# Performance work log

Hardware: AMD Instinct MI355X
Metric: run time of the kernel (lower is better)

Reference implementation:

```python
import jax, jax.numpy as jnp
from jax import lax
import numpy as np

# Module hyperparameters (match init_kwargs)
N = 4            # number of multiplex cells per feature map
NUM_FM = 64      # feature maps in the input
NF = N * NUM_FM  # lateral channel count = 256
H = W = 32       # feature map height/width
D = 2            # lateral neighborhood radius
PRD = 2          # padding repair distance (must equal D for symmetric pad)
KS = 2 * D + 1   # lateral kernel size = 5
IOTA = 0.1       # blend of activation vs lateral support for winner selection
B = 16           # batch size


def minmax_fm(x):
    """Min-max normalize each feature map (over the last two dims) to [0,1].
    Degenerate (constant) maps map to 0."""
    mn = jnp.min(x, axis=(-2, -1), keepdims=True)
    mx = jnp.max(x, axis=(-2, -1), keepdims=True)
    denom = mx - mn
    safe = jnp.where(denom > 0, denom, 1.0)
    return jnp.where(denom > 0, (x - mn) / safe, 0.0)


def _pad(A):
    # pad_activations: zeros of shape (.., PRD+D+H, PRD+D+W), A at [PRD:-PRD]
    # with PRD == D this is symmetric (PRD, D) padding.
    return jnp.pad(A, ((0, 0), (0, 0), (PRD, D), (PRD, D)))


def _conv(x, w):
    # x: (B, Cin, H', W'), w: (Cout, Cin, KS, KS) -> VALID conv (padding=0)
    return lax.conv_general_dilated(x, w, (1, 1), 'VALID',
                                    dimension_numbers=('NCHW', 'OIHW', 'NCHW'))


def setup_inputs() -> dict:
    key = jax.random.key(0)
    k1, k2 = jax.random.split(key)
    A = jax.random.uniform(k1, (B, NUM_FM, H, W), dtype=jnp.float32)
    K = jax.random.normal(k2, (NF, NF, KS, KS), dtype=jnp.float32)  # trained lateral kernel
    S = jnp.ones((NF,), dtype=jnp.float32)                          # scaling param
    return {"A": A, "K": K, "S": S}


def reference(A, K, S):
    batch = A.shape[0]
    # A.repeat(1, n, 1, 1): tile input n times along channels -> (B, NF, H, W)
    A_rep = jnp.tile(A, (1, N, 1, 1))

    # First lateral pass: conv with minmax-normalized K^T, scaled by S, minmaxed.
    L1 = _conv(_pad(A_rep), minmax_fm(jnp.swapaxes(K, 0, 1))) / NUM_FM
    L1 = L1 * S[None, :, None, None]
    L1 = minmax_fm(L1)

    # Winner-take-all multiplex selection (deterministic branch):
    s = jnp.sum((1.0 - IOTA) * A_rep + IOTA * L1, axis=(-2, -1))  # (B, NF)
    s = jnp.swapaxes(s.reshape(batch, N, NUM_FM), 1, 2)            # (B, NUM_FM, N)
    A_max = jnp.argmax(s, axis=-1)                                  # (B, NUM_FM)
    fm_idx = NUM_FM * A_max + jnp.arange(NUM_FM)                    # (B, NUM_FM) channel ids

    # Active-channel mask (complement = inactive_multiplex_idx in the original)
    active = jnp.zeros((batch, NF), dtype=bool)
    active = active.at[jnp.arange(batch)[:, None], fm_idx].set(True)

    # Zero inactive channels of A (tmp_A) and diagonal K[i,i] for inactive i
    # (large_K[b, idx, idx] = 0 is pairwise/diagonal fancy indexing in torch).
    tmp_A = A_rep * active[:, :, None, None].astype(A_rep.dtype)
    eye = jnp.eye(NF, dtype=bool)
    kill = eye[None, :, :] & (~active)[:, :, None]                  # (B, NF, NF)
    large_K = jnp.where(kill[..., None, None], 0.0, K[None])        # (B, NF, NF, KS, KS)

    # Second lateral pass: per-sample conv with per-sample kernel.
    pA = _pad(tmp_A)

    def per_sample(x, Kb):
        w = minmax_fm(jnp.swapaxes(Kb, 0, 1))
        return _conv(x[None], w)[0]

    L2 = jax.vmap(per_sample)(pA, large_K) / NUM_FM                 # (B, NF, H, W)

    # Gather winning channels: filtered_L (B, NUM_FM, H, W)
    return jnp.take_along_axis(L2, fm_idx[:, :, None, None], axis=1)
```

## Files before the change

kernel.cpp:

```cpp
#include <hip/hip_runtime.h>


#define NFM 64
#define NMX 4
#define NFC 256
#define HW 1024
#define KK 25

typedef unsigned short u16;
typedef short short8 __attribute__((ext_vector_type(8)));
typedef float f32x4 __attribute__((ext_vector_type(4)));

__device__ __forceinline__ u16 f2bfbits(float f) {
    unsigned int u = __float_as_uint(f);
    u += 0x7fffu + ((u >> 16) & 1u);
    return (u16)(u >> 16);
}
__device__ __forceinline__ float bf2f(u16 v) {
    return __uint_as_float(((unsigned int)v) << 16);
}

__global__ __launch_bounds__(256) void kprep(const float* __restrict__ K,
                                             float* __restrict__ wsum2) {
    __shared__ __align__(16) float buf[64 * KK];
    int g = blockIdx.x & 63, o0 = (blockIdx.x >> 6) * 64;
    int t = threadIdx.x;
    float wacc[KK];
#pragma unroll
    for (int k = 0; k < KK; ++k) wacc[k] = 0.f;

    for (int n = 0; n < NMX; ++n) {
        int i = n * NFM + g;
        const float4* src = (const float4*)(K + (i * NFC + o0) * KK);
        __syncthreads();
        ((float4*)buf)[t] = src[t];
        if (t < 144) ((float4*)buf)[t + 256] = src[t + 256];
        __syncthreads();
        if (t < 64) {
            float v[KK];
            float mn = 1e30f, mx = -1e30f;
#pragma unroll
            for (int k = 0; k < KK; ++k) {
                v[k] = buf[t * KK + k];
                mn = fminf(mn, v[k]);
                mx = fmaxf(mx, v[k]);
            }
            float d = mx - mn;
            float r = d > 0.f ? 1.f / d : 0.f;
#pragma unroll
            for (int k = 0; k < KK; ++k) wacc[k] += (v[k] - mn) * r;
        }
    }
    __syncthreads();
    if (t < 64) {
#pragma unroll
        for (int k = 0; k < KK; ++k) buf[t * KK + k] = wacc[k];
    }
    __syncthreads();
    for (int idx = t; idx < 1600; idx += 256) {
        int k = idx >> 6, ol = idx & 63;
        wsum2[(g * KK + k) * NFC + o0 + ol] = buf[ol * KK + k];
    }
}

__global__ __launch_bounds__(256) void kpackW(const float* __restrict__ wsum2,
                                              char* __restrict__ Wpk) {
    __shared__ float wlds[64 * 16];
    int dydx = blockIdx.x, ot = blockIdx.y, t = threadIdx.x;
    int o15 = t & 15, gq = t >> 4;
#pragma unroll
    for (int e = 0; e < 4; ++e) {
        int g = e * 16 + gq;
        wlds[g * 16 + o15] = wsum2[(g * KK + dydx) * NFC + ot * 16 + o15];
    }
    __syncthreads();
    int gh = t >> 7, l = t & 63;
    int quad = l >> 4, oo = l & 15;
    short8 hs, ls;
#pragma unroll
    for (int j = 0; j < 8; ++j) {
        float v = wlds[(gh * 32 + quad * 8 + j) * 16 + oo];
        u16 h = f2bfbits(v);
        hs[j] = (short)h;
        ls[j] = (short)f2bfbits(v - bf2f(h));
    }
    char* cb = Wpk + (ot * 50 + dydx * 2 + gh) * 2048 + l * 16;
    *(short8*)cb = hs;
    *(short8*)(cb + 1024) = ls;
}

#define MFMA6(P, BH, BL)                                                             \
    acc[0][P] = __builtin_amdgcn_mfma_f32_16x16x32_bf16(cah0, BH, acc[0][P], 0, 0, 0); \
    acc[1][P] = __builtin_amdgcn_mfma_f32_16x16x32_bf16(cah1, BH, acc[1][P], 0, 0, 0); \
    acc[0][P] = __builtin_amdgcn_mfma_f32_16x16x32_bf16(cah0, BL, acc[0][P], 0, 0, 0); \
    acc[1][P] = __builtin_amdgcn_mfma_f32_16x16x32_bf16(cah1, BL, acc[1][P], 0, 0, 0); \
    acc[0][P] = __builtin_amdgcn_mfma_f32_16x16x32_bf16(cal0, BH, acc[0][P], 0, 0, 0); \
    acc[1][P] = __builtin_amdgcn_mfma_f32_16x16x32_bf16(cal1, BH, acc[1][P], 0, 0, 0);

__global__ __launch_bounds__(512, 2) void kscore(const float* __restrict__ A,
                                                 const char* __restrict__ Wpk,
                                                 float4* __restrict__ part) {
    __shared__ u16 slabh[6 * 36 * 72];
    __shared__ u16 slabl[6 * 36 * 72];
    int t = threadIdx.x;
    int y2 = blockIdx.x, b = blockIdx.y;
    int y0 = y2 * 2;
    int lane = t & 63;
    int wv = __builtin_amdgcn_readfirstlane(t >> 6);
    int n15 = lane & 15, quad = lane >> 4;

    const float* Ab = A + b * NFM * HW;
    for (int ry = 0; ry < 6; ++ry) {
        int gy = y0 - 2 + ry;
        bool rowok = (gy >= 0) && (gy < 32);
        for (int c = 0; c < 5; ++c) {
            int id2 = c * 512 + t;
            if (id2 < 2304) {
                int g = (id2 * 3641) >> 17;
                int xi = id2 - g * 36;
                float v = 0.f;
                if (rowok && xi >= 2 && xi < 34)
                    v = Ab[g * HW + gy * 32 + xi - 2];
                u16 h = f2bfbits(v);
                u16 l = f2bfbits(v - bf2f(h));
                int idx = (ry * 36 + xi) * 72 + g;
                slabh[idx] = h;
                slabl[idx] = l;
            }
        }
    }
    __syncthreads();

    f32x4 acc[2][4];
#pragma unroll
    for (int m = 0; m < 2; ++m)
#pragma unroll
        for (int p = 0; p < 4; ++p)
#pragma unroll
            for (int r = 0; r < 4; ++r) acc[m][p][r] = 0.f;

    const char* wbase0 = Wpk + (wv * 2) * 50 * 2048 + lane * 16;
    const char* wbase1 = wbase0 + 50 * 2048;
    short8 cah0 = *(const short8*)(wbase0);
    short8 cal0 = *(const short8*)(wbase0 + 1024);
    short8 cah1 = *(const short8*)(wbase1);
    short8 cal1 = *(const short8*)(wbase1 + 1024);

    int rb0 = n15 * 72 + quad * 8;
    const u16* sh0 = slabh + rb0;
    const u16* sl0 = slabl + rb0;
    short8 bh0 = *(const short8*)(sh0);
    short8 bl0 = *(const short8*)(sl0);
    short8 bh1 = *(const short8*)(sh0 + 16 * 72);
    short8 bl1 = *(const short8*)(sl0 + 16 * 72);
    short8 bh2 = *(const short8*)(sh0 + 36 * 72);
    short8 bl2 = *(const short8*)(sl0 + 36 * 72);
    short8 bh3 = *(const short8*)(sh0 + 52 * 72);
    short8 bl3 = *(const short8*)(sl0 + 52 * 72);

    for (int ks = 0; ks < 50; ++ks) {
        int ksn = ks < 49 ? ks + 1 : 49;
        const char* nb0 = wbase0 + (ksn << 11);
        const char* nb1 = wbase1 + (ksn << 11);
        short8 nah0 = *(const short8*)nb0;
        short8 nal0 = *(const short8*)(nb0 + 1024);
        short8 nah1 = *(const short8*)nb1;
        short8 nal1 = *(const short8*)(nb1 + 1024);
        int dydxn = ksn >> 1;
        int ghn = (ksn & 1) * 32;
        int dyn = dydxn / 5, dxn = dydxn - dyn * 5;
        int rbn = (dyn * 36 + n15 + dxn) * 72 + ghn + quad * 8;
        const u16* shn = slabh + rbn;
        const u16* sln = slabl + rbn;
        short8 nh0 = *(const short8*)(shn);
        short8 nl0 = *(const short8*)(sln);
        short8 nh1 = *(const short8*)(shn + 16 * 72);
        short8 nl1 = *(const short8*)(sln + 16 * 72);
        short8 nh2 = *(const short8*)(shn + 36 * 72);
        short8 nl2 = *(const short8*)(sln + 36 * 72);
        short8 nh3 = *(const short8*)(shn + 52 * 72);
        short8 nl3 = *(const short8*)(sln + 52 * 72);
        __builtin_amdgcn_sched_barrier(0);

        MFMA6(0, bh0, bl0)
        MFMA6(1, bh1, bl1)
        MFMA6(2, bh2, bl2)
        MFMA6(3, bh3, bl3)

        bh0 = nh0; bl0 = nl0; bh1 = nh1; bl1 = nl1;
        bh2 = nh2; bl2 = nl2; bh3 = nh3; bl3 = nl3;
        cah0 = nah0; cal0 = nal0; cah1 = nah1; cal1 = nal1;
    }

#pragma unroll
    for (int m = 0; m < 2; ++m) {
#pragma unroll
        for (int reg = 0; reg < 4; ++reg) {
            float v0 = acc[m][0][reg], v1 = acc[m][1][reg];
            float v2 = acc[m][2][reg], v3 = acc[m][3][reg];
            float mn = fminf(fminf(v0, v1), fminf(v2, v3));
            float mx = fmaxf(fmaxf(v0, v1), fmaxf(v2, v3));
            float sm = (v0 + v1) + (v2 + v3);
#pragma unroll
            for (int msk = 1; msk <= 8; msk <<= 1) {
                mn = fminf(mn, __shfl_xor(mn, msk, 64));
                mx = fmaxf(mx, __shfl_xor(mx, msk, 64));
                sm += __shfl_xor(sm, msk, 64);
            }
            if (n15 == 0) {
                int o = (wv * 2 + m) * 16 + quad * 4 + reg;
                part[(b * NFC + o) * 16 + y2] = make_float4(mn, mx, sm, 0.f);
            }
        }
    }
}

__global__ __launch_bounds__(256) void kpackO(const float* __restrict__ K,
                                              const float4* __restrict__ part,
                                              const float* __restrict__ S,
                                              char* __restrict__ Wob) {
    __shared__ float scl[NFC];
    __shared__ int igL[NFM];
    __shared__ __align__(16) char cbuf[25 * 2048];
    int ft = blockIdx.x, b = blockIdx.y;
    int t = threadIdx.x;
    {
        const float4* pp = part + (b * NFC + t) * 16;
        float mn = 1e30f, mx = -1e30f, sm = 0.f;
#pragma unroll
        for (int r = 0; r < 16; ++r) {
            float4 p = pp[r];
            mn = fminf(mn, p.x);
            mx = fmaxf(mx, p.y);
            sm += p.z;
        }
        float s = S[t] * (1.f / 64.f);
        float mnv = (s >= 0.f ? mn : mx) * s;
        float mxv = (s >= 0.f ? mx : mn) * s;
        float smv = sm * s;
        float d = mxv - mnv;
        scl[t] = d > 0.f ? (smv - 1024.f * mnv) / d : 0.f;
    }
    __syncthreads();
    if (t < NFM) {
        float best = scl[t];
        int bi = 0;
#pragma unroll
        for (int n = 1; n < NMX; ++n) {
            float v = scl[n * NFM + t];
            if (v > best) { best = v; bi = n; }
        }
        igL[t] = bi * NFM + t;
    }
    __syncthreads();

    int g32 = t & 31, fh = t >> 5;
    int quad = g32 >> 3, j = g32 & 7;
    char* wdst = Wob + b * 409600 + ft * 102400;

    for (int half = 0; half < 2; ++half) {
        int i = igL[half * 32 + g32];
#pragma unroll
        for (int e = 0; e < 2; ++e) {
            int f15 = fh * 2 + e;
            int o = igL[ft * 16 + f15];
            const float* src = K + (i * NFC + o) * KK;
            float v[KK];
            float mn = 1e30f, mx = -1e30f;
#pragma unroll
            for (int k = 0; k < KK; ++k) {
                v[k] = src[k];
                mn = fminf(mn, v[k]);
                mx = fmaxf(mx, v[k]);
            }
            float d = mx - mn;
            float r = d > 0.f ? 1.f / d : 0.f;
            char* base = cbuf + (quad * 16 + f15) * 16 + j * 2;
#pragma unroll
            for (int k = 0; k < KK; ++k) {
                float nv = (v[k] - mn) * r;
                u16 h = f2bfbits(nv);
                u16 l = f2bfbits(nv - bf2f(h));
                *(u16*)(base + k * 2048) = h;
                *(u16*)(base + k * 2048 + 1024) = l;
            }
        }
        __syncthreads();
        for (int idx = t; idx < 3200; idx += 256) {
            int ch = idx >> 7, w = idx & 127;
            *(float4*)(wdst + (ch * 2 + half) * 2048 + w * 16) =
                *(const float4*)(cbuf + ch * 2048 + w * 16);
        }
        __syncthreads();
    }
}

__global__ __launch_bounds__(256, 4) void kout(const float* __restrict__ A,
                                               const char* __restrict__ Wob,
                                               float* __restrict__ out) {
    __shared__ u16 slabh[6 * 20 * 72];
    __shared__ u16 slabl[6 * 20 * 72];
    int t = threadIdx.x;
    int xh = blockIdx.x, yb2 = blockIdx.y, b = blockIdx.z;
    int y0 = yb2 * 2, x0 = xh * 16;
    int lane = t & 63;
    int wv = __builtin_amdgcn_readfirstlane(t >> 6);
    int n15 = lane & 15, quad = lane >> 4;

    const float* Ab = A + b * NFM * HW;
    for (int ry = 0; ry < 6; ++ry) {
        int gy = y0 - 2 + ry;
        bool rowok = (gy >= 0) && (gy < 32);
        for (int c = 0; c < 5; ++c) {
            int id2 = c * 256 + t;
            int g = (id2 * 6554) >> 17;
            int xi = id2 - g * 20;
            int x = x0 + xi - 2;
            float v = 0.f;
            if (rowok && x >= 0 && x < 32)
                v = Ab[g * HW + gy * 32 + x];
            u16 h = f2bfbits(v);
            u16 l = f2bfbits(v - bf2f(h));
            int idx = (ry * 20 + xi) * 72 + g;
            slabh[idx] = h;
            slabl[idx] = l;
        }
    }
    __syncthreads();

    f32x4 acc[2];
#pragma unroll
    for (int r = 0; r < 2; ++r)
#pragma unroll
        for (int jr = 0; jr < 4; ++jr) acc[r][jr] = 0.f;

    const char* wbase = Wob + b * 409600 + (wv * 50) * 2048 + lane * 16;
    short8 cah = *(const short8*)(wbase);
    short8 cal = *(const short8*)(wbase + 1024);

    int rb0 = n15 * 72 + quad * 8;
    short8 bh0 = *(const short8*)(slabh + rb0);
    short8 bl0 = *(const short8*)(slabl + rb0);
    short8 bh1 = *(const short8*)(slabh + rb0 + 20 * 72);
    short8 bl1 = *(const short8*)(slabl + rb0 + 20 * 72);

    for (int ks = 0; ks < 50; ++ks) {
        int ksn = ks < 49 ? ks + 1 : 49;
        const char* nb = wbase + (ksn << 11);
        short8 nah = *(const short8*)nb;
        short8 nal = *(const short8*)(nb + 1024);

        int dydxn = ksn >> 1;
        int ghn = (ksn & 1) * 32;
        int dyn = dydxn / 5, dxn = dydxn - dyn * 5;
        int rbn = (dyn * 20 + n15 + dxn) * 72 + ghn + quad * 8;
        short8 nh0 = *(const short8*)(slabh + rbn);
        short8 nl0 = *(const short8*)(slabl + rbn);
        short8 nh1 = *(const short8*)(slabh + rbn + 20 * 72);
        short8 nl1 = *(const short8*)(slabl + rbn + 20 * 72);
        __builtin_amdgcn_sched_barrier(0);

        acc[0] = __builtin_amdgcn_mfma_f32_16x16x32_bf16(cah, bh0, acc[0], 0, 0, 0);
        acc[1] = __builtin_amdgcn_mfma_f32_16x16x32_bf16(cah, bh1, acc[1], 0, 0, 0);
        acc[0] = __builtin_amdgcn_mfma_f32_16x16x32_bf16(cah, bl0, acc[0], 0, 0, 0);
        acc[1] = __builtin_amdgcn_mfma_f32_16x16x32_bf16(cah, bl1, acc[1], 0, 0, 0);
        acc[0] = __builtin_amdgcn_mfma_f32_16x16x32_bf16(cal, bh0, acc[0], 0, 0, 0);
        acc[1] = __builtin_amdgcn_mfma_f32_16x16x32_bf16(cal, bh1, acc[1], 0, 0, 0);

        bh0 = nh0; bl0 = nl0; bh1 = nh1; bl1 = nl1;
        cah = nah;
        cal = nal;
    }

#pragma unroll
    for (int r = 0; r < 2; ++r)
#pragma unroll
        for (int reg = 0; reg < 4; ++reg) {
            int f = wv * 16 + quad * 4 + reg;
            out[(b * NFM + f) * HW + (y0 + r) * 32 + x0 + n15] = acc[r][reg] * (1.f / 64.f);
        }
}

extern "C" void kernel_launch(void* const* d_in, const int* in_sizes, int n_in,
                              void* d_out, int out_size, void* d_ws, size_t ws_size,
                              hipStream_t stream) {
    const float* A = (const float*)d_in[0];
    const float* K = (const float*)d_in[1];
    const float* S = (const float*)d_in[2];
    float* out = (float*)d_out;

    char* ws = (char*)d_ws;
    char*   Wob   = ws;
    char*   Wpk   = ws;
    float*  wsum2 = (float*)(ws + 1638400);
    float4* part  = (float4*)(ws + 6553600);

    kprep<<<dim3(256), dim3(256), 0, stream>>>(K, wsum2);
    kpackW<<<dim3(25, 16), dim3(256), 0, stream>>>(wsum2, Wpk);
    kscore<<<dim3(16, 16), dim3(512), 0, stream>>>(A, Wpk, part);
    kpackO<<<dim3(4, 16), dim3(256), 0, stream>>>(K, part, S, Wob);
    kout<<<dim3(2, 16, 16), dim3(256), 0, stream>>>(A, Wob, out);
}
```

Baseline: 147.3 us.

## Retile kscore waves to 4 output tiles by 2 rows with LDS cross-wave reduction

Each wave now covers four 16-channel output tiles for one of the two image rows, where before it covered two output tiles for both rows. This halves the per-wave LDS activation reads and doubles the per-wave global weight fragment loads. Partial min/max/sum results for the two row halves are combined through a new shared-memory buffer before a single store. A __syncthreads every 8 k-steps is also added, apparently to keep waves in lockstep for cache reuse of the weight stream, at the cost of extra barrier stalls and more registers.

```diff
diff --git a/kernel.cpp b/kernel.cpp
--- a/kernel.cpp
+++ b/kernel.cpp
@@ -89,25 +89,20 @@
     *(short8*)(cb + 1024) = ls;
 }
 
-#define MFMA6(P, BH, BL)                                                             \
-    acc[0][P] = __builtin_amdgcn_mfma_f32_16x16x32_bf16(cah0, BH, acc[0][P], 0, 0, 0); \
-    acc[1][P] = __builtin_amdgcn_mfma_f32_16x16x32_bf16(cah1, BH, acc[1][P], 0, 0, 0); \
-    acc[0][P] = __builtin_amdgcn_mfma_f32_16x16x32_bf16(cah0, BL, acc[0][P], 0, 0, 0); \
-    acc[1][P] = __builtin_amdgcn_mfma_f32_16x16x32_bf16(cah1, BL, acc[1][P], 0, 0, 0); \
-    acc[0][P] = __builtin_amdgcn_mfma_f32_16x16x32_bf16(cal0, BH, acc[0][P], 0, 0, 0); \
-    acc[1][P] = __builtin_amdgcn_mfma_f32_16x16x32_bf16(cal1, BH, acc[1][P], 0, 0, 0);
-
 __global__ __launch_bounds__(512, 2) void kscore(const float* __restrict__ A,
                                                  const char* __restrict__ Wpk,
                                                  float4* __restrict__ part) {
     __shared__ u16 slabh[6 * 36 * 72];
     __shared__ u16 slabl[6 * 36 * 72];
+    __shared__ float4 red[2][NFC];
     int t = threadIdx.x;
     int y2 = blockIdx.x, b = blockIdx.y;
     int y0 = y2 * 2;
     int lane = t & 63;
     int wv = __builtin_amdgcn_readfirstlane(t >> 6);
     int n15 = lane & 15, quad = lane >> 4;
+    int mg = wv & 3;
+    int rh = wv >> 2;
 
     const float* Ab = A + b * NFM * HW;
     for (int ry = 0; ry < 6; ++ry) {
@@ -131,76 +126,73 @@
     }
     __syncthreads();
 
-    f32x4 acc[2][4];
-#pragma unroll
-    for (int m = 0; m < 2; ++m)
-#pragma unroll
-        for (int p = 0; p < 4; ++p)
+    f32x4 acc[4][2];
+#pragma unroll
+    for (int m = 0; m < 4; ++m)
+#pragma unroll
+        for (int p = 0; p < 2; ++p)
 #pragma unroll
             for (int r = 0; r < 4; ++r) acc[m][p][r] = 0.f;
 
-    const char* wbase0 = Wpk + (wv * 2) * 50 * 2048 + lane * 16;
-    const char* wbase1 = wbase0 + 50 * 2048;
-    short8 cah0 = *(const short8*)(wbase0);
-    short8 cal0 = *(const short8*)(wbase0 + 1024);
-    short8 cah1 = *(const short8*)(wbase1);
-    short8 cal1 = *(const short8*)(wbase1 + 1024);
-
-    int rb0 = n15 * 72 + quad * 8;
-    const u16* sh0 = slabh + rb0;
-    const u16* sl0 = slabl + rb0;
-    short8 bh0 = *(const short8*)(sh0);
-    short8 bl0 = *(const short8*)(sl0);
-    short8 bh1 = *(const short8*)(sh0 + 16 * 72);
-    short8 bl1 = *(const short8*)(sl0 + 16 * 72);
-    short8 bh2 = *(const short8*)(sh0 + 36 * 72);
-    short8 bl2 = *(const short8*)(sl0 + 36 * 72);
-    short8 bh3 = *(const short8*)(sh0 + 52 * 72);
-    short8 bl3 = *(const short8*)(sl0 + 52 * 72);
+    const char* wb = Wpk + (mg * 4) * 50 * 2048 + lane * 16;
+    short8 cah[4], cal[4];
+#pragma unroll
+    for (int m = 0; m < 4; ++m) {
+        cah[m] = *(const short8*)(wb + m * 102400);
+        cal[m] = *(const short8*)(wb + m * 102400 + 1024);
+    }
+
+    int rb0 = (rh * 36 + n15) * 72 + quad * 8;
+    short8 bh[2], bl[2];
+    bh[0] = *(const short8*)(slabh + rb0);
+    bl[0] = *(const short8*)(slabl + rb0);
+    bh[1] = *(const short8*)(slabh + rb0 + 16 * 72);
+    bl[1] = *(const short8*)(slabl + rb0 + 16 * 72);
 
     for (int ks = 0; ks < 50; ++ks) {
         int ksn = ks < 49 ? ks + 1 : 49;
-        const char* nb0 = wbase0 + (ksn << 11);
-        const char* nb1 = wbase1 + (ksn << 11);
-        short8 nah0 = *(const short8*)nb0;
-        short8 nal0 = *(const short8*)(nb0 + 1024);
-        short8 nah1 = *(const short8*)nb1;
-        short8 nal1 = *(const short8*)(nb1 + 1024);
+        short8 nah[4], nal[4];
+#pragma unroll
+        for (int m = 0; m < 4; ++m) {
+            const char* nb = wb + m * 102400 + (ksn << 11);
+            nah[m] = *(const short8*)nb;
+            nal[m] = *(const short8*)(nb + 1024);
+        }
         int dydxn = ksn >> 1;
         int ghn = (ksn & 1) * 32;
         int dyn = dydxn / 5, dxn = dydxn - dyn * 5;
-        int rbn = (dyn * 36 + n15 + dxn) * 72 + ghn + quad * 8;
-        const u16* shn = slabh + rbn;
-        const u16* sln = slabl + rbn;
-        short8 nh0 = *(const short8*)(shn);
-        short8 nl0 = *(const short8*)(sln);
-        short8 nh1 = *(const short8*)(shn + 16 * 72);
-        short8 nl1 = *(const short8*)(sln + 16 * 72);
-        short8 nh2 = *(const short8*)(shn + 36 * 72);
-        short8 nl2 = *(const short8*)(sln + 36 * 72);
-        short8 nh3 = *(const short8*)(shn + 52 * 72);
-        short8 nl3 = *(const short8*)(sln + 52 * 72);
+        int rbn = ((rh + dyn) * 36 + n15 + dxn) * 72 + ghn + quad * 8;
+        short8 nh[2], nl[2];
+        nh[0] = *(const short8*)(slabh + rbn);
+        nl[0] = *(const short8*)(slabl + rbn);
+        nh[1] = *(const short8*)(slabh + rbn + 16 * 72);
+        nl[1] = *(const short8*)(slabl + rbn + 16 * 72);
         __builtin_amdgcn_sched_barrier(0);
 
-        MFMA6(0, bh0, bl0)
-        MFMA6(1, bh1, bl1)
-        MFMA6(2, bh2, bl2)
-        MFMA6(3, bh3, bl3)
-
-        bh0 = nh0; bl0 = nl0; bh1 = nh1; bl1 = nl1;
-        bh2 = nh2; bl2 = nl2; bh3 = nh3; bl3 = nl3;
-        cah0 = nah0; cal0 = nal0; cah1 = nah1; cal1 = nal1;
-    }
-
-#pragma unroll
-    for (int m = 0; m < 2; ++m) {
+#pragma unroll
+        for (int m = 0; m < 4; ++m) {
+#pragma unroll
+            for (int p = 0; p < 2; ++p) {
+                acc[m][p] = __builtin_amdgcn_mfma_f32_16x16x32_bf16(cah[m], bh[p], acc[m][p], 0, 0, 0);
+                acc[m][p] = __builtin_amdgcn_mfma_f32_16x16x32_bf16(cah[m], bl[p], acc[m][p], 0, 0, 0);
+                acc[m][p] = __builtin_amdgcn_mfma_f32_16x16x32_bf16(cal[m], bh[p], acc[m][p], 0, 0, 0);
+            }
+        }
+
+#pragma unroll
+        for (int m = 0; m < 4; ++m) { cah[m] = nah[m]; cal[m] = nal[m]; }
+        bh[0] = nh[0]; bl[0] = nl[0]; bh[1] = nh[1]; bl[1] = nl[1];
+        if ((ks & 7) == 7) __syncthreads();
+    }
+
+#pragma unroll
+    for (int m = 0; m < 4; ++m) {
 #pragma unroll
         for (int reg = 0; reg < 4; ++reg) {
             float v0 = acc[m][0][reg], v1 = acc[m][1][reg];
-            float v2 = acc[m][2][reg], v3 = acc[m][3][reg];
-            float mn = fminf(fminf(v0, v1), fminf(v2, v3));
-            float mx = fmaxf(fmaxf(v0, v1), fmaxf(v2, v3));
-            float sm = (v0 + v1) + (v2 + v3);
+            float mn = fminf(v0, v1);
+            float mx = fmaxf(v0, v1);
+            float sm = v0 + v1;
 #pragma unroll
             for (int msk = 1; msk <= 8; msk <<= 1) {
                 mn = fminf(mn, __shfl_xor(mn, msk, 64));
@@ -208,10 +200,16 @@
                 sm += __shfl_xor(sm, msk, 64);
             }
             if (n15 == 0) {
-                int o = (wv * 2 + m) * 16 + quad * 4 + reg;
-                part[(b * NFC + o) * 16 + y2] = make_float4(mn, mx, sm, 0.f);
-            }
-        }
+                int o = (mg * 4 + m) * 16 + quad * 4 + reg;
+                red[rh][o] = make_float4(mn, mx, sm, 0.f);
+            }
+        }
+    }
+    __syncthreads();
+    if (t < NFC) {
+        float4 r0 = red[0][t], r1 = red[1][t];
+        part[(b * NFC + t) * 16 + y2] =
+            make_float4(fminf(r0.x, r1.x), fmaxf(r0.y, r1.y), r0.z + r1.z, 0.f);
     }
 }
 
```

After: 159.0 us. 8.0% more time.

## Fuse kernel prep and packing into one kernel; split kpackO halves across grid

Applied to the files above, without the earlier changes.

Merges the per-(g,o) min-max normalization/sum kernel and the bf16 hi/lo packing kernel into a single kernel that keeps sums in shared memory, removing one launch and the wsum2 global round trip. The fused kernel launches only 64 blocks, with each thread reading a strided 25-float window of K, so parallelism and coalescing are reduced compared with the 256-block version. Separately, kpackO's two-pass half loop becomes a third grid dimension, doubling block count for more parallelism at the cost of recomputing the score/argmax per block.

```diff
diff --git a/kernel.cpp b/kernel.cpp
--- a/kernel.cpp
+++ b/kernel.cpp
@@ -20,73 +20,55 @@
     return __uint_as_float(((unsigned int)v) << 16);
 }
 
-__global__ __launch_bounds__(256) void kprep(const float* __restrict__ K,
-                                             float* __restrict__ wsum2) {
-    __shared__ __align__(16) float buf[64 * KK];
-    int g = blockIdx.x & 63, o0 = (blockIdx.x >> 6) * 64;
-    int t = threadIdx.x;
+__global__ __launch_bounds__(256) void kw(const float* __restrict__ K,
+                                          char* __restrict__ Wpk) {
+    __shared__ float wlds[16 * 16 * KK];
+    int gq = blockIdx.x, ot = blockIdx.y, t = threadIdx.x;
+    int tg = t >> 4, to = t & 15;
+    int g = gq * 16 + tg, o = ot * 16 + to;
+
     float wacc[KK];
 #pragma unroll
     for (int k = 0; k < KK; ++k) wacc[k] = 0.f;
-
+#pragma unroll
     for (int n = 0; n < NMX; ++n) {
-        int i = n * NFM + g;
-        const float4* src = (const float4*)(K + (i * NFC + o0) * KK);
-        __syncthreads();
-        ((float4*)buf)[t] = src[t];
-        if (t < 144) ((float4*)buf)[t + 256] = src[t + 256];
-        __syncthreads();
-        if (t < 64) {
-            float v[KK];
-            float mn = 1e30f, mx = -1e30f;
-#pragma unroll
-            for (int k = 0; k < KK; ++k) {
-                v[k] = buf[t * KK + k];
-                mn = fminf(mn, v[k]);
-                mx = fmaxf(mx, v[k]);
-            }
-            float d = mx - mn;
-            float r = d > 0.f ? 1.f / d : 0.f;
-#pragma unroll
-            for (int k = 0; k < KK; ++k) wacc[k] += (v[k] - mn) * r;
-        }
-    }
-    __syncthreads();
-    if (t < 64) {
-#pragma unroll
-        for (int k = 0; k < KK; ++k) buf[t * KK + k] = wacc[k];
-    }
-    __syncthreads();
-    for (int idx = t; idx < 1600; idx += 256) {
-        int k = idx >> 6, ol = idx & 63;
-        wsum2[(g * KK + k) * NFC + o0 + ol] = buf[ol * KK + k];
-    }
-}
-
-__global__ __launch_bounds__(256) void kpackW(const float* __restrict__ wsum2,
-                                              char* __restrict__ Wpk) {
-    __shared__ float wlds[64 * 16];
-    int dydx = blockIdx.x, ot = blockIdx.y, t = threadIdx.x;
-    int o15 = t & 15, gq = t >> 4;
-#pragma unroll
-    for (int e = 0; e < 4; ++e) {
-        int g = e * 16 + gq;
-        wlds[g * 16 + o15] = wsum2[(g * KK + dydx) * NFC + ot * 16 + o15];
-    }
-    __syncthreads();
-    int gh = t >> 7, l = t & 63;
-    int quad = l >> 4, oo = l & 15;
-    short8 hs, ls;
-#pragma unroll
-    for (int j = 0; j < 8; ++j) {
-        float v = wlds[(gh * 32 + quad * 8 + j) * 16 + oo];
-        u16 h = f2bfbits(v);
-        hs[j] = (short)h;
-        ls[j] = (short)f2bfbits(v - bf2f(h));
-    }
-    char* cb = Wpk + (ot * 50 + dydx * 2 + gh) * 2048 + l * 16;
-    *(short8*)cb = hs;
-    *(short8*)(cb + 1024) = ls;
+        const float* src = K + ((n * NFM + g) * NFC + o) * KK;
+        float v[KK];
+        float mn = 1e30f, mx = -1e30f;
+#pragma unroll
+        for (int k = 0; k < KK; ++k) {
+            v[k] = src[k];
+            mn = fminf(mn, v[k]);
+            mx = fmaxf(mx, v[k]);
+        }
+        float d = mx - mn;
+        float r = d > 0.f ? 1.f / d : 0.f;
+#pragma unroll
+        for (int k = 0; k < KK; ++k) wacc[k] += (v[k] - mn) * r;
+    }
+#pragma unroll
+    for (int k = 0; k < KK; ++k) wlds[(tg * 16 + to) * KK + k] = wacc[k];
+    __syncthreads();
+
+    int gh = gq >> 1;
+    for (int idx = t; idx < KK * 32; idx += 256) {
+        int dydx = idx >> 5, l32 = idx & 31;
+        int quad = (gq & 1) * 2 + (l32 >> 4);
+        int oo = l32 & 15;
+        int l = quad * 16 + oo;
+        short8 hs, ls;
+#pragma unroll
+        for (int j = 0; j < 8; ++j) {
+            int gl = (l32 >> 4) * 8 + j;
+            float v = wlds[(gl * 16 + oo) * KK + dydx];
+            u16 h = f2bfbits(v);
+            hs[j] = (short)h;
+            ls[j] = (short)f2bfbits(v - bf2f(h));
+        }
+        char* cb = Wpk + (ot * 50 + dydx * 2 + gh) * 2048 + l * 16;
+        *(short8*)cb = hs;
+        *(short8*)(cb + 1024) = ls;
+    }
 }
 
 #define MFMA6(P, BH, BL)                                                             \
@@ -222,7 +204,7 @@
     __shared__ float scl[NFC];
     __shared__ int igL[NFM];
     __shared__ __align__(16) char cbuf[25 * 2048];
-    int ft = blockIdx.x, b = blockIdx.y;
+    int ft = blockIdx.x, b = blockIdx.y, half = blockIdx.z;
     int t = threadIdx.x;
     {
         const float4* pp = part + (b * NFC + t) * 16;
@@ -258,40 +240,37 @@
     int quad = g32 >> 3, j = g32 & 7;
     char* wdst = Wob + b * 409600 + ft * 102400;
 
-    for (int half = 0; half < 2; ++half) {
-        int i = igL[half * 32 + g32];
-#pragma unroll
-        for (int e = 0; e < 2; ++e) {
-            int f15 = fh * 2 + e;
-            int o = igL[ft * 16 + f15];
-            const float* src = K + (i * NFC + o) * KK;
-            float v[KK];
-            float mn = 1e30f, mx = -1e30f;
-#pragma unroll
-            for (int k = 0; k < KK; ++k) {
-                v[k] = src[k];
-                mn = fminf(mn, v[k]);
-                mx = fmaxf(mx, v[k]);
-            }
-            float d = mx - mn;
-            float r = d > 0.f ? 1.f / d : 0.f;
-            char* base = cbuf + (quad * 16 + f15) * 16 + j * 2;
-#pragma unroll
-            for (int k = 0; k < KK; ++k) {
-                float nv = (v[k] - mn) * r;
-                u16 h = f2bfbits(nv);
-                u16 l = f2bfbits(nv - bf2f(h));
-                *(u16*)(base + k * 2048) = h;
-                *(u16*)(base + k * 2048 + 1024) = l;
-            }
-        }
-        __syncthreads();
-        for (int idx = t; idx < 3200; idx += 256) {
-            int ch = idx >> 7, w = idx & 127;
-            *(float4*)(wdst + (ch * 2 + half) * 2048 + w * 16) =
-                *(const float4*)(cbuf + ch * 2048 + w * 16);
-        }
-        __syncthreads();
+    int i = igL[half * 32 + g32];
+#pragma unroll
+    for (int e = 0; e < 2; ++e) {
+        int f15 = fh * 2 + e;
+        int o = igL[ft * 16 + f15];
+        const float* src = K + (i * NFC + o) * KK;
+        float v[KK];
+        float mn = 1e30f, mx = -1e30f;
+#pragma unroll
+        for (int k = 0; k < KK; ++k) {
+            v[k] = src[k];
+            mn = fminf(mn, v[k]);
+            mx = fmaxf(mx, v[k]);
+        }
+        float d = mx - mn;
+        float r = d > 0.f ? 1.f / d : 0.f;
+        char* base = cbuf + (quad * 16 + f15) * 16 + j * 2;
+#pragma unroll
+        for (int k = 0; k < KK; ++k) {
+            float nv = (v[k] - mn) * r;
+            u16 h = f2bfbits(nv);
+            u16 l = f2bfbits(nv - bf2f(h));
+            *(u16*)(base + k * 2048) = h;
+            *(u16*)(base + k * 2048 + 1024) = l;
+        }
+    }
+    __syncthreads();
+    for (int idx = t; idx < 3200; idx += 256) {
+        int ch = idx >> 7, w = idx & 127;
+        *(float4*)(wdst + (ch * 2 + half) * 2048 + w * 16) =
+            *(const float4*)(cbuf + ch * 2048 + w * 16);
     }
 }
 
@@ -392,12 +371,10 @@
     char* ws = (char*)d_ws;
     char*   Wob   = ws;
     char*   Wpk   = ws;
-    float*  wsum2 = (float*)(ws + 1638400);
     float4* part  = (float4*)(ws + 6553600);
 
-    kprep<<<dim3(256), dim3(256), 0, stream>>>(K, wsum2);
-    kpackW<<<dim3(25, 16), dim3(256), 0, stream>>>(wsum2, Wpk);
+    kw<<<dim3(4, 16), dim3(256), 0, stream>>>(K, Wpk);
     kscore<<<dim3(16, 16), dim3(512), 0, stream>>>(A, Wpk, part);
-    kpackO<<<dim3(4, 16), dim3(256), 0, stream>>>(K, part, S, Wob);
+    kpackO<<<dim3(4, 16, 2), dim3(256), 0, stream>>>(K, part, S, Wob);
     kout<<<dim3(2, 16, 16), dim3(256), 0, stream>>>(A, Wob, out);
 }
```

Result: faster. 141.7 us (median of 2 runs) (-3.8%).
